# Kernel optimization log

Measured on AMD Instinct MI355X. Metric: run time of the kernel, lower is better.

Reference implementation:

```python
import jax, jax.numpy as jnp
import numpy as np

H = 128            # hidden_size; also the chunk length from torch.split(x, hidden_size)
NUM_CHUNKS = 4096  # B
INPUT_SIZE = 1
NUM_CLASSES = 1


def setup_inputs() -> dict:
    key = jax.random.key(0)
    ks = jax.random.split(key, 7)
    N = NUM_CHUNKS * H
    s = 1.0 / np.sqrt(H).astype(np.float32)
    x = jax.random.normal(ks[0], (N,), dtype=jnp.float32)
    W_ih = jax.random.uniform(ks[1], (4 * H, INPUT_SIZE), minval=-s, maxval=s, dtype=jnp.float32)
    W_hh = jax.random.uniform(ks[2], (4 * H, H), minval=-s, maxval=s, dtype=jnp.float32)
    b_ih = jax.random.uniform(ks[3], (4 * H,), minval=-s, maxval=s, dtype=jnp.float32)
    b_hh = jax.random.uniform(ks[4], (4 * H,), minval=-s, maxval=s, dtype=jnp.float32)
    fc_W = jax.random.uniform(ks[5], (NUM_CLASSES, H), minval=-s, maxval=s, dtype=jnp.float32)
    fc_b = jax.random.uniform(ks[6], (NUM_CLASSES,), minval=-s, maxval=s, dtype=jnp.float32)
    return {"x": x, "W_ih": W_ih, "W_hh": W_hh, "b_ih": b_ih, "b_hh": b_hh,
            "fc_W": fc_W, "fc_b": fc_b}


def reference(x, W_ih, W_hh, b_ih, b_hh, fc_W, fc_b):
    # Original: split flat x into chunks of length H, run each chunk as a
    # batch-1 LSTM (input_size=1), take final hidden state, apply fc_out.
    # Here all chunks are batched into one fused recurrent pass.
    Hh = W_hh.shape[1]
    xb = x.reshape(-1, Hh, 1)                                  # [B, T=H, 1]
    # input projection is time-parallel: precompute gate pre-activations
    pre = jnp.einsum('bti,gi->btg', xb, W_ih) + b_ih + b_hh    # [B, T, 4H]

    def step(carry, p_t):
        h, c = carry                                           # [B, H] each
        gates = p_t + h @ W_hh.T                               # [B, 4H]
        i, f, g, o = jnp.split(gates, 4, axis=-1)              # PyTorch gate order i,f,g,o
        i = jax.nn.sigmoid(i)
        f = jax.nn.sigmoid(f)
        g = jnp.tanh(g)
        o = jax.nn.sigmoid(o)
        c = f * c + i * g
        h = o * jnp.tanh(c)
        return (h, c), None

    B = xb.shape[0]
    h0 = jnp.zeros((B, Hh), dtype=x.dtype)
    c0 = jnp.zeros((B, Hh), dtype=x.dtype)
    (hT, _), _ = jax.lax.scan(step, (h0, c0), jnp.swapaxes(pre, 0, 1))
    return hT @ fc_W.T + fc_b                                  # [B, num_classes]
```

## Files before the change

kernel.cpp:

```cpp
#include <hip/hip_runtime.h>


#define H   128
#define T   128
#define BLOCK 512
#define HSTRIDE 136
#define XSTRIDE 20
#define LOG2E    1.44269504088896340736f
#define TWOLOG2E 2.88539008177792681472f

typedef _Float16 f16x8 __attribute__((ext_vector_type(8)));
typedef float    f32x4 __attribute__((ext_vector_type(4)));

__global__ void prep_whh_kernel(const float* __restrict__ W_hh, _Float16* __restrict__ wfrag)
{
    int idx = blockIdx.x * blockDim.x + threadIdx.x;
    int l15 =  idx        & 15;
    int q   = (idx >> 4)  & 3;
    int kc  = (idx >> 6)  & 3;
    int g   = (idx >> 8)  & 3;
    int ct  = (idx >> 10) & 7;
    int n  = g * H + ct * 16 + l15;
    int k0 = kc * 32 + q * 8;
    float s = (g == 2) ? TWOLOG2E : LOG2E;
    const float* src = W_hh + (size_t)n * H + k0;
    f16x8 f;
    #pragma unroll
    for (int i = 0; i < 8; ++i) f[i] = (_Float16)(src[i] * s);
    *(f16x8*)(wfrag + (size_t)idx * 8) = f;
}

__device__ __forceinline__ float frcp(float v)  { return __builtin_amdgcn_rcpf(v); }
__device__ __forceinline__ float fexp2(float v) { return __builtin_amdgcn_exp2f(v); }

__device__ __forceinline__ void lstm_step(const _Float16* hr, _Float16* hw,
                                          f32x4 iv[4], const float* xp_next,
                                          const f16x8 wf[4][4],
                                          const float* wihs, const float* biass,
                                          float* c, int l15, int q, int jcol)
{
    const _Float16* ar = hr + l15 * HSTRIDE + q * 8;
    f16x8 af0 = *(const f16x8*)(ar);
    f16x8 af1 = *(const f16x8*)(ar + 32);
    f16x8 af2 = *(const f16x8*)(ar + 64);
    f16x8 af3 = *(const f16x8*)(ar + 96);

    const f32x4 zz = {0.f, 0.f, 0.f, 0.f};
    f32x4 lo[4], hi[4];
    #pragma unroll
    for (int g = 0; g < 4; ++g)
        lo[g] = __builtin_amdgcn_mfma_f32_16x16x32_f16(af0, wf[g][0], iv[g], 0, 0, 0);
    #pragma unroll
    for (int g = 0; g < 4; ++g)
        hi[g] = __builtin_amdgcn_mfma_f32_16x16x32_f16(af2, wf[g][2], zz, 0, 0, 0);
    #pragma unroll
    for (int g = 0; g < 4; ++g)
        lo[g] = __builtin_amdgcn_mfma_f32_16x16x32_f16(af1, wf[g][1], lo[g], 0, 0, 0);
    #pragma unroll
    for (int g = 0; g < 4; ++g)
        hi[g] = __builtin_amdgcn_mfma_f32_16x16x32_f16(af3, wf[g][3], hi[g], 0, 0, 0);

    {
        float4 xl = *(const float4*)xp_next;
        #pragma unroll
        for (int g = 0; g < 4; ++g) {
            iv[g][0] = fmaf(xl.x, wihs[g], biass[g]);
            iv[g][1] = fmaf(xl.y, wihs[g], biass[g]);
            iv[g][2] = fmaf(xl.z, wihs[g], biass[g]);
            iv[g][3] = fmaf(xl.w, wihs[g], biass[g]);
        }
    }

    f32x4 acc[4];
    #pragma unroll
    for (int g = 0; g < 4; ++g)
        acc[g] = lo[g] + hi[g];

    float Ei[4], Ef[4], Eg[4], Eo[4];
    #pragma unroll
    for (int r = 0; r < 4; ++r) {
        Ei[r] = fexp2(-acc[0][r]);
        Ef[r] = fexp2(-acc[1][r]);
        Eg[r] = fexp2( acc[2][r]);
        Eo[r] = fexp2(-acc[3][r]);
    }
    _Float16* hwp = hw + (q * 4) * HSTRIDE + jcol;
    #pragma unroll
    for (int r = 0; r < 4; ++r) {
        float u  = 1.0f + Ei[r];
        float v  = 1.0f + Ef[r];
        float w  = 1.0f + Eg[r];
        float wm = Eg[r] - 1.0f;
        float uw = u * w;
        float cn = fmaf(c[r], uw, wm * v) * frcp(v * uw);
        c[r] = cn;
        float Ec = fexp2(cn * TWOLOG2E);
        float hv = (Ec - 1.0f) * frcp((Ec + 1.0f) * (1.0f + Eo[r]));
        hwp[r * HSTRIDE] = (_Float16)hv;
    }
}

__launch_bounds__(BLOCK, 2)
__global__ void lstm_fused_kernel(const float* __restrict__ x,
                                  const float* __restrict__ W_ih,
                                  const _Float16* __restrict__ wfrag,
                                  const float* __restrict__ b_ih,
                                  const float* __restrict__ b_hh,
                                  const float* __restrict__ fc_W,
                                  const float* __restrict__ fc_b,
                                  float* __restrict__ out)
{
    __shared__ __align__(16) float xs[T + 1][XSTRIDE];
    __shared__ __align__(16) _Float16 hb0[16 * HSTRIDE];
    __shared__ __align__(16) _Float16 hb1[16 * HSTRIDE];

    const int tid  = threadIdx.x;
    const int wave = tid >> 6;
    const int lane = tid & 63;
    const int l15  = lane & 15;
    const int q    = lane >> 4;
    const int jcol = wave * 16 + l15;

    {
        const int t0 = tid & 127;
        const int bb = tid >> 7;
        const float* xb = x + (size_t)blockIdx.x * (16 * T);
        xs[t0][bb]      = xb[bb * T + t0];
        xs[t0][bb + 4]  = xb[(bb + 4) * T + t0];
        xs[t0][bb + 8]  = xb[(bb + 8) * T + t0];
        xs[t0][bb + 12] = xb[(bb + 12) * T + t0];
    }
    for (int i = tid; i < 16 * HSTRIDE; i += BLOCK)
        hb0[i] = (_Float16)0.0f;

    f16x8 wf[4][4];
    float wihs[4], biass[4];
    {
        const _Float16* wbase = wfrag + (size_t)wave * 8192;
        #pragma unroll
        for (int g = 0; g < 4; ++g) {
            const int n = g * H + jcol;
            const float s = (g == 2) ? TWOLOG2E : LOG2E;
            wihs[g]  = W_ih[n] * s;
            biass[g] = (b_ih[n] + b_hh[n]) * s;
            #pragma unroll
            for (int kc = 0; kc < 4; ++kc)
                wf[g][kc] = *(const f16x8*)(wbase + ((((g * 4 + kc) * 4 + q) * 16 + l15) * 8));
        }
    }

    float c[4] = {0.f, 0.f, 0.f, 0.f};

    __syncthreads();

    f32x4 iv[4];
    {
        float4 xl = *(const float4*)&xs[0][q * 4];
        #pragma unroll
        for (int g = 0; g < 4; ++g) {
            iv[g][0] = fmaf(xl.x, wihs[g], biass[g]);
            iv[g][1] = fmaf(xl.y, wihs[g], biass[g]);
            iv[g][2] = fmaf(xl.z, wihs[g], biass[g]);
            iv[g][3] = fmaf(xl.w, wihs[g], biass[g]);
        }
    }
    const float* xpn = &xs[1][q * 4];

    #pragma unroll 1
    for (int t2 = 0; t2 < T / 2; ++t2) {
        lstm_step(hb0, hb1, iv, xpn, wf, wihs, biass, c, l15, q, jcol);
        xpn += XSTRIDE;
        __syncthreads();
        lstm_step(hb1, hb0, iv, xpn, wf, wihs, biass, c, l15, q, jcol);
        xpn += XSTRIDE;
        __syncthreads();
    }

    if (tid < 256) {
        const int b    = tid >> 4;
        const int part = tid & 15;
        const _Float16* hrow = &hb0[b * HSTRIDE];
        float s = 0.0f;
        #pragma unroll
        for (int i = 0; i < 8; ++i) {
            const int j = part * 8 + i;
            s += fc_W[j] * (float)hrow[j];
        }
        s += __shfl_xor(s, 8, 16);
        s += __shfl_xor(s, 4, 16);
        s += __shfl_xor(s, 2, 16);
        s += __shfl_xor(s, 1, 16);
        if (part == 0)
            out[blockIdx.x * 16 + b] = s + fc_b[0];
    }
}

extern "C" void kernel_launch(void* const* d_in, const int* in_sizes, int n_in,
                              void* d_out, int out_size, void* d_ws, size_t ws_size,
                              hipStream_t stream)
{
    const float* x    = (const float*)d_in[0];
    const float* W_ih = (const float*)d_in[1];
    const float* W_hh = (const float*)d_in[2];
    const float* b_ih = (const float*)d_in[3];
    const float* b_hh = (const float*)d_in[4];
    const float* fc_W = (const float*)d_in[5];
    const float* fc_b = (const float*)d_in[6];
    float* out = (float*)d_out;

    _Float16* wfrag = (_Float16*)d_ws;

    hipLaunchKernelGGL(prep_whh_kernel, dim3(32), dim3(256), 0, stream, W_hh, wfrag);

    const int B = in_sizes[0] / H;
    dim3 grid(B / 16);
    dim3 block(BLOCK);
    hipLaunchKernelGGL(lstm_fused_kernel, grid, block, 0, stream,
                       x, W_ih, wfrag, b_ih, b_hh, fc_W, fc_b, out);
}
```

Baseline: 169.0 us.

## Transpose MFMA operands, drop W_hh prep kernel, vectorize gate math and h stores

Swaps the A/B operands of the MFMA so each lane's accumulator holds four hidden units of one batch row, which allows a single packed f16x4 store of h per lane instead of four strided scalar stores. The separate prep kernel that converted W_hh to fp16 fragments is removed; each block now loads and converts W_hh from fp32 global memory directly into registers. Gate math is reorganized into float2 vectors to encourage packed FP32 ops, and the x term is broadcast per lane. This removes a kernel launch and scattered LDS writes, at the cost of every block redundantly reading fp32 W_hh at startup.

```diff
diff --git a/kernel.cpp b/kernel.cpp
--- a/kernel.cpp
+++ b/kernel.cpp
@@ -10,34 +10,19 @@
 #define TWOLOG2E 2.88539008177792681472f
 
 typedef _Float16 f16x8 __attribute__((ext_vector_type(8)));
+typedef _Float16 f16x4 __attribute__((ext_vector_type(4)));
 typedef float    f32x4 __attribute__((ext_vector_type(4)));
-
-__global__ void prep_whh_kernel(const float* __restrict__ W_hh, _Float16* __restrict__ wfrag)
-{
-    int idx = blockIdx.x * blockDim.x + threadIdx.x;
-    int l15 =  idx        & 15;
-    int q   = (idx >> 4)  & 3;
-    int kc  = (idx >> 6)  & 3;
-    int g   = (idx >> 8)  & 3;
-    int ct  = (idx >> 10) & 7;
-    int n  = g * H + ct * 16 + l15;
-    int k0 = kc * 32 + q * 8;
-    float s = (g == 2) ? TWOLOG2E : LOG2E;
-    const float* src = W_hh + (size_t)n * H + k0;
-    f16x8 f;
-    #pragma unroll
-    for (int i = 0; i < 8; ++i) f[i] = (_Float16)(src[i] * s);
-    *(f16x8*)(wfrag + (size_t)idx * 8) = f;
-}
+typedef float    f32x2 __attribute__((ext_vector_type(2)));
 
 __device__ __forceinline__ float frcp(float v)  { return __builtin_amdgcn_rcpf(v); }
 __device__ __forceinline__ float fexp2(float v) { return __builtin_amdgcn_exp2f(v); }
 
-__device__ __forceinline__ void lstm_step(const _Float16* hr, _Float16* hw,
+__device__ __forceinline__ void lstm_step(const _Float16* __restrict__ hr,
+                                          _Float16* __restrict__ hw,
                                           f32x4 iv[4], const float* xp_next,
                                           const f16x8 wf[4][4],
-                                          const float* wihs, const float* biass,
-                                          float* c, int l15, int q, int jcol)
+                                          const f32x4 wihv[4], const f32x4 biasv[4],
+                                          f32x2 C[2], int l15, int q, int hcol0)
 {
     const _Float16* ar = hr + l15 * HSTRIDE + q * 8;
     f16x8 af0 = *(const f16x8*)(ar);
@@ -49,26 +34,23 @@
     f32x4 lo[4], hi[4];
     #pragma unroll
     for (int g = 0; g < 4; ++g)
-        lo[g] = __builtin_amdgcn_mfma_f32_16x16x32_f16(af0, wf[g][0], iv[g], 0, 0, 0);
-    #pragma unroll
-    for (int g = 0; g < 4; ++g)
-        hi[g] = __builtin_amdgcn_mfma_f32_16x16x32_f16(af2, wf[g][2], zz, 0, 0, 0);
-    #pragma unroll
-    for (int g = 0; g < 4; ++g)
-        lo[g] = __builtin_amdgcn_mfma_f32_16x16x32_f16(af1, wf[g][1], lo[g], 0, 0, 0);
-    #pragma unroll
-    for (int g = 0; g < 4; ++g)
-        hi[g] = __builtin_amdgcn_mfma_f32_16x16x32_f16(af3, wf[g][3], hi[g], 0, 0, 0);
+        lo[g] = __builtin_amdgcn_mfma_f32_16x16x32_f16(wf[g][0], af0, iv[g], 0, 0, 0);
+    #pragma unroll
+    for (int g = 0; g < 4; ++g)
+        hi[g] = __builtin_amdgcn_mfma_f32_16x16x32_f16(wf[g][2], af2, zz, 0, 0, 0);
+    #pragma unroll
+    for (int g = 0; g < 4; ++g)
+        lo[g] = __builtin_amdgcn_mfma_f32_16x16x32_f16(wf[g][1], af1, lo[g], 0, 0, 0);
+    #pragma unroll
+    for (int g = 0; g < 4; ++g)
+        hi[g] = __builtin_amdgcn_mfma_f32_16x16x32_f16(wf[g][3], af3, hi[g], 0, 0, 0);
 
     {
-        float4 xl = *(const float4*)xp_next;
-        #pragma unroll
-        for (int g = 0; g < 4; ++g) {
-            iv[g][0] = fmaf(xl.x, wihs[g], biass[g]);
-            iv[g][1] = fmaf(xl.y, wihs[g], biass[g]);
-            iv[g][2] = fmaf(xl.z, wihs[g], biass[g]);
-            iv[g][3] = fmaf(xl.w, wihs[g], biass[g]);
-        }
+        float xv = xp_next[l15];
+        f32x4 xb = {xv, xv, xv, xv};
+        #pragma unroll
+        for (int g = 0; g < 4; ++g)
+            iv[g] = __builtin_elementwise_fma(xb, wihv[g], biasv[g]);
     }
 
     f32x4 acc[4];
@@ -76,34 +58,45 @@
     for (int g = 0; g < 4; ++g)
         acc[g] = lo[g] + hi[g];
 
-    float Ei[4], Ef[4], Eg[4], Eo[4];
-    #pragma unroll
-    for (int r = 0; r < 4; ++r) {
-        Ei[r] = fexp2(-acc[0][r]);
-        Ef[r] = fexp2(-acc[1][r]);
-        Eg[r] = fexp2( acc[2][r]);
-        Eo[r] = fexp2(-acc[3][r]);
-    }
-    _Float16* hwp = hw + (q * 4) * HSTRIDE + jcol;
-    #pragma unroll
-    for (int r = 0; r < 4; ++r) {
-        float u  = 1.0f + Ei[r];
-        float v  = 1.0f + Ef[r];
-        float w  = 1.0f + Eg[r];
-        float wm = Eg[r] - 1.0f;
-        float uw = u * w;
-        float cn = fmaf(c[r], uw, wm * v) * frcp(v * uw);
-        c[r] = cn;
-        float Ec = fexp2(cn * TWOLOG2E);
-        float hv = (Ec - 1.0f) * frcp((Ec + 1.0f) * (1.0f + Eo[r]));
-        hwp[r * HSTRIDE] = (_Float16)hv;
-    }
+    f32x2 Ei[2], Ef[2], Eg[2], Eo[2];
+    #pragma unroll
+    for (int p = 0; p < 2; ++p) {
+        Ei[p] = (f32x2){ fexp2(-acc[0][2 * p]), fexp2(-acc[0][2 * p + 1]) };
+        Ef[p] = (f32x2){ fexp2(-acc[1][2 * p]), fexp2(-acc[1][2 * p + 1]) };
+        Eg[p] = (f32x2){ fexp2( acc[2][2 * p]), fexp2( acc[2][2 * p + 1]) };
+        Eo[p] = (f32x2){ fexp2(-acc[3][2 * p]), fexp2(-acc[3][2 * p + 1]) };
+    }
+
+    const f32x2 one2 = {1.0f, 1.0f};
+    const f32x2 k2   = { TWOLOG2E,  TWOLOG2E};
+    const f32x2 mk2  = {-TWOLOG2E, -TWOLOG2E};
+    f16x4 hh;
+    #pragma unroll
+    for (int p = 0; p < 2; ++p) {
+        f32x2 u  = one2 + Ei[p];
+        f32x2 v  = one2 + Ef[p];
+        f32x2 w  = one2 + Eg[p];
+        f32x2 wm = __builtin_elementwise_fma(Eg[p], k2, mk2);
+        f32x2 uw = u * w;
+        f32x2 nm = __builtin_elementwise_fma(C[p], uw, wm * v);
+        f32x2 dn = v * uw;
+        f32x2 rd = { frcp(dn[0]), frcp(dn[1]) };
+        f32x2 cn = nm * rd;
+        C[p] = cn;
+        f32x2 ec  = { fexp2(cn[0]), fexp2(cn[1]) };
+        f32x2 den = (ec + one2) * (one2 + Eo[p]);
+        f32x2 rh  = { frcp(den[0]), frcp(den[1]) };
+        f32x2 hv  = (ec - one2) * rh;
+        hh[2 * p]     = (_Float16)hv[0];
+        hh[2 * p + 1] = (_Float16)hv[1];
+    }
+    *(f16x4*)(hw + l15 * HSTRIDE + hcol0) = hh;
 }
 
 __launch_bounds__(BLOCK, 2)
 __global__ void lstm_fused_kernel(const float* __restrict__ x,
                                   const float* __restrict__ W_ih,
-                                  const _Float16* __restrict__ wfrag,
+                                  const float* __restrict__ W_hh,
                                   const float* __restrict__ b_ih,
                                   const float* __restrict__ b_hh,
                                   const float* __restrict__ fc_W,
@@ -119,7 +112,7 @@
     const int lane = tid & 63;
     const int l15  = lane & 15;
     const int q    = lane >> 4;
-    const int jcol = wave * 16 + l15;
+    const int hcol0 = wave * 16 + q * 4;
 
     {
         const int t0 = tid & 127;
@@ -134,44 +127,50 @@
         hb0[i] = (_Float16)0.0f;
 
     f16x8 wf[4][4];
-    float wihs[4], biass[4];
-    {
-        const _Float16* wbase = wfrag + (size_t)wave * 8192;
-        #pragma unroll
-        for (int g = 0; g < 4; ++g) {
-            const int n = g * H + jcol;
-            const float s = (g == 2) ? TWOLOG2E : LOG2E;
-            wihs[g]  = W_ih[n] * s;
-            biass[g] = (b_ih[n] + b_hh[n]) * s;
-            #pragma unroll
-            for (int kc = 0; kc < 4; ++kc)
-                wf[g][kc] = *(const f16x8*)(wbase + ((((g * 4 + kc) * 4 + q) * 16 + l15) * 8));
+    f32x4 wihv[4], biasv[4];
+    #pragma unroll
+    for (int g = 0; g < 4; ++g) {
+        const float s = (g == 2) ? TWOLOG2E : LOG2E;
+        #pragma unroll
+        for (int kc = 0; kc < 4; ++kc) {
+            const float* src = W_hh + (size_t)(g * H + wave * 16 + l15) * H + kc * 32 + q * 8;
+            float4 w0 = *(const float4*)src;
+            float4 w1 = *(const float4*)(src + 4);
+            f16x8 f;
+            f[0] = (_Float16)(w0.x * s); f[1] = (_Float16)(w0.y * s);
+            f[2] = (_Float16)(w0.z * s); f[3] = (_Float16)(w0.w * s);
+            f[4] = (_Float16)(w1.x * s); f[5] = (_Float16)(w1.y * s);
+            f[6] = (_Float16)(w1.z * s); f[7] = (_Float16)(w1.w * s);
+            wf[g][kc] = f;
         }
-    }
-
-    float c[4] = {0.f, 0.f, 0.f, 0.f};
+        #pragma unroll
+        for (int r = 0; r < 4; ++r) {
+            const int n = g * H + hcol0 + r;
+            wihv[g][r]  = W_ih[n] * s;
+            biasv[g][r] = (b_ih[n] + b_hh[n]) * s;
+        }
+    }
+
+    f32x2 C[2] = {{0.f, 0.f}, {0.f, 0.f}};
 
     __syncthreads();
 
     f32x4 iv[4];
     {
-        float4 xl = *(const float4*)&xs[0][q * 4];
-        #pragma unroll
-        for (int g = 0; g < 4; ++g) {
-            iv[g][0] = fmaf(xl.x, wihs[g], biass[g]);
-            iv[g][1] = fmaf(xl.y, wihs[g], biass[g]);
-            iv[g][2] = fmaf(xl.z, wihs[g], biass[g]);
-            iv[g][3] = fmaf(xl.w, wihs[g], biass[g]);
-        }
-    }
-    const float* xpn = &xs[1][q * 4];
+        float xv = xs[0][l15];
+        f32x4 xb = {xv, xv, xv, xv};
+        #pragma unroll
+        for (int g = 0; g < 4; ++g)
+            iv[g] = __builtin_elementwise_fma(xb, wihv[g], biasv[g]);
+    }
+    const float* xpn = &xs[1][0];
 
     #pragma unroll 1
     for (int t2 = 0; t2 < T / 2; ++t2) {
-        lstm_step(hb0, hb1, iv, xpn, wf, wihs, biass, c, l15, q, jcol);
+        lstm_step(hb0, hb1, iv, xpn, wf, wihv, biasv, C, l15, q, hcol0);
         xpn += XSTRIDE;
         __syncthreads();
-        lstm_step(hb1, hb0, iv, xpn, wf, wihs, biass, c, l15, q, jcol);
+        lstm_step(hb1, hb0, iv, xpn, wf, wihv, biasv, C, l15, q, hcol0);
         xpn += XSTRIDE;
         __syncthreads();
     }
@@ -207,14 +206,11 @@
     const float* fc_W = (const float*)d_in[5];
     const float* fc_b = (const float*)d_in[6];
     float* out = (float*)d_out;
-
-    _Float16* wfrag = (_Float16*)d_ws;
-
-    hipLaunchKernelGGL(prep_whh_kernel, dim3(32), dim3(256), 0, stream, W_hh, wfrag);
+    (void)d_ws; (void)ws_size;
 
     const int B = in_sizes[0] / H;
     dim3 grid(B / 16);
     dim3 block(BLOCK);
     hipLaunchKernelGGL(lstm_fused_kernel, grid, block, 0, stream,
-                       x, W_ih, wfrag, b_ih, b_hh, fc_W, fc_b, out);
+                       x, W_ih, W_hh, b_ih, b_hh, fc_W, fc_b, out);
 }
```

Result: faster. 158.4 us (-6.3%).
